# Kernel tuning notes

Measured on AMD Instinct MI355X. Metric: run time of the kernel, lower is better.

The kernel has to match this reference:

```python
import math
import jax, jax.numpy as jnp
import numpy as np

BS, N, D, H = 4, 512, 1024, 16
HD = D // H


def setup_inputs() -> dict:
    key = jax.random.key(0)
    ks = jax.random.split(key, 12)
    s = 1.0 / math.sqrt(D)
    return {
        "x": jax.random.normal(ks[0], (BS, N, D), jnp.float32),
        "r": jax.random.normal(ks[1], (BS, 3, N, N), jnp.float32),
        "bias": jax.random.normal(ks[2], (BS, H, N, N), jnp.float32),
        "mask": jax.random.randint(ks[3], (BS, 1, N, N), 0, 2, jnp.int32),
        "wq": jax.random.normal(ks[4], (D, D), jnp.float32) * s,
        "bq": jnp.zeros((D,), jnp.float32),
        "wk": jax.random.normal(ks[5], (D, D), jnp.float32) * s,
        "bk": jnp.zeros((D,), jnp.float32),
        "wv": jax.random.normal(ks[6], (D, D), jnp.float32) * s,
        "bv": jnp.zeros((D,), jnp.float32),
        "wo": jax.random.normal(ks[7], (D, 1), jnp.float32) * s,
        "bo": jnp.zeros((1,), jnp.float32),
    }


def reference(x, r, bias, mask, wq, bq, wk, bk, wv, bv, wo, bo):
    bs, n, d = x.shape
    # projections -> (bs, h, n, hd)
    q = (x @ wq + bq).reshape(bs, n, H, HD).transpose(0, 2, 1, 3)
    k = (x @ wk + bk).reshape(bs, n, H, HD).transpose(0, 2, 1, 3)
    v = (x @ wv + bv).reshape(bs, n, H, HD).transpose(0, 2, 1, 3)
    logits = jnp.einsum("bhid,bhjd->bhij", q, k) / math.sqrt(HD) + bias
    logits = jnp.where(mask == 0, jnp.float32(-1e9), logits)
    w = jax.nn.softmax(logits, axis=-1)  # (bs,h,n,n)
    # o[b,i,c,h,d] = sum_j r[b,c,i,j] * w[b,h,i,j] * v[b,h,j,d]
    o = jnp.einsum("bcij,bhij,bhjd->bichd", r, w, v)
    o = o.reshape(bs, n, 3, d)
    force = o @ wo + bo  # (bs, n, 3, 1)
    return force
```

## Files before the change

### kernel.cpp

```cpp
#include <hip/hip_runtime.h>
#include <stdint.h>

#define BSZ 4
#define NSEQ 512
#define DMOD 1024
#define NH 16
#define HD 64

typedef __attribute__((ext_vector_type(8))) short bf16x8;
typedef __attribute__((ext_vector_type(4))) float f32x4;

__device__ __forceinline__ unsigned short f2bf(float f) {
    union { float f; uint32_t u; } v; v.f = f;
    uint32_t u = v.u;
    u += 0x7FFFu + ((u >> 16) & 1u);
    return (unsigned short)(u >> 16);
}

__device__ __forceinline__ void gload_lds16(const unsigned short* g, unsigned short* l) {
    __builtin_amdgcn_global_load_lds(
        (const __attribute__((address_space(1))) void*)g,
        (__attribute__((address_space(3))) void*)l, 16, 0, 0);
}

__global__ __launch_bounds__(256) void k_prep(
        const float* __restrict__ x, const float* __restrict__ wq, const float* __restrict__ wk,
        const float* __restrict__ wv, const float* __restrict__ bv, const float* __restrict__ wo,
        unsigned short* __restrict__ xb, unsigned short* __restrict__ wqt,
        unsigned short* __restrict__ wkt, float* __restrict__ wv2t, float* __restrict__ bv2) {
    __shared__ float t[32][33];
    int bx = blockIdx.x, tid = threadIdx.x;
    if (bx < 2048) {
        int i = bx * 256 + tid;
        float4 v = ((const float4*)x)[i];
        ushort4 o; o.x = f2bf(v.x); o.y = f2bf(v.y); o.z = f2bf(v.z); o.w = f2bf(v.w);
        ((ushort4*)xb)[i] = o;
    } else if (bx < 4096) {
        int g = bx - 2048; int z = g >> 10; g &= 1023;
        const float* src = z ? wk : wq;
        unsigned short* dst = z ? wkt : wqt;
        int be = (g & 31) * 32, bc = (g >> 5) * 32;
        int tx = tid & 31, ty = tid >> 5;
        #pragma unroll
        for (int yy = 0; yy < 32; yy += 8)
            t[ty + yy][tx] = src[(size_t)(be + ty + yy) * DMOD + bc + tx];
        __syncthreads();
        #pragma unroll
        for (int yy = 0; yy < 32; yy += 8)
            dst[(size_t)(bc + ty + yy) * DMOD + be + tx] = f2bf(t[tx][ty + yy]);
    } else {
        int g = bx - 4096;
        int grp = tid >> 6, l = tid & 63;
        int e = g * 4 + grp;
        float out = 0.f;
        #pragma unroll
        for (int it = 0; it < 16; ++it) {
            float v = wv[(size_t)e * DMOD + it * 64 + l] * wo[it * 64 + l];
            #pragma unroll
            for (int off = 1; off < 64; off <<= 1) v += __shfl_xor(v, off, 64);
            if (l == it) out = v;
        }
        if (l < 16) wv2t[l * DMOD + e] = out;
        if (g == 0 && grp == 0) {
            float ob = 0.f;
            #pragma unroll
            for (int it = 0; it < 16; ++it) {
                float v = bv[it * 64 + l] * wo[it * 64 + l];
                #pragma unroll
                for (int off = 1; off < 64; off <<= 1) v += __shfl_xor(v, off, 64);
                if (l == it) ob = v;
            }
            if (l < 16) bv2[l] = ob;
        }
    }
}

__global__ __launch_bounds__(256) void k_mid(
        const float* __restrict__ x, const float* __restrict__ wv2t, const float* __restrict__ bv2,
        const unsigned short* __restrict__ xb, const unsigned short* __restrict__ wqt,
        const unsigned short* __restrict__ wkt, const float* __restrict__ bq,
        const float* __restrict__ bk, float* __restrict__ u,
        unsigned short* __restrict__ qT, unsigned short* __restrict__ kT) {
    __shared__ unsigned short lA[64 * 128];
    __shared__ unsigned short lB[64 * 128];
    int bx = blockIdx.x, tid = threadIdx.x;
    if (bx < 512) {
        int wave = bx * 4 + (tid >> 6);
        int l = tid & 63;
        int b = wave >> 9, j = wave & 511;
        const float* xr = x + (size_t)(b * NSEQ + j) * DMOD;
        float p[16];
        #pragma unroll
        for (int h = 0; h < 16; ++h) p[h] = 0.f;
        for (int it = 0; it < 16; ++it) {
            int e = l + it * 64;
            float xv = xr[e];
            #pragma unroll
            for (int h = 0; h < 16; ++h) p[h] += xv * wv2t[h * DMOD + e];
        }
        #pragma unroll
        for (int h = 0; h < 16; ++h) {
            #pragma unroll
            for (int off = 1; off < 64; off <<= 1) p[h] += __shfl_xor(p[h], off, 64);
        }
        float out = 0.f;
        #pragma unroll
        for (int h = 0; h < 16; ++h) if (l == h) out = p[h] + bv2[h];
        if (l < 16) u[(b * 16 + l) * NSEQ + j] = out;
        return;
    }
    int g = bx - 512;
    int z = g >> 9;
    const unsigned short* Wt = z ? wkt : wqt;
    const float* bias = z ? bk : bq;
    unsigned short* outT = z ? kT : qT;
    float scale = z ? 1.f : 0.125f;
    int w = tid >> 6, lane = tid & 63;
    int quad = lane >> 4, col = lane & 15;
    int m0 = (g & 31) * 64;
    int n0 = ((g >> 5) & 15) * 64;

    f32x4 acc[4];
    #pragma unroll
    for (int nt = 0; nt < 4; ++nt) acc[nt] = (f32x4){0.f, 0.f, 0.f, 0.f};

    int rl_base = lane >> 4;
    int cs = lane & 15;
    int asw = cs & 7;

    for (int kc = 0; kc < 8; ++kc) {
        int k0 = kc * 128;
        #pragma unroll
        for (int t = 0; t < 4; ++t) {
            int rl = t * 4 + rl_base;
            int row = w * 16 + rl;
            int cg = cs ^ (rl & 7);
            gload_lds16(xb + (size_t)(m0 + row) * DMOD + k0 + cg * 8,
                        &lA[(w * 16 + t * 4) * 128]);
            gload_lds16(Wt + (size_t)(n0 + row) * DMOD + k0 + cg * 8,
                        &lB[(w * 16 + t * 4) * 128]);
        }
        __syncthreads();
        int arow = w * 16 + cs;
        #pragma unroll
        for (int ks = 0; ks < 4; ++ks) {
            int blk = (ks * 4 + quad) ^ asw;
            bf16x8 af = *(const bf16x8*)&lA[arow * 128 + blk * 8];
            #pragma unroll
            for (int nt = 0; nt < 4; ++nt) {
                bf16x8 bfr = *(const bf16x8*)&lB[(nt * 16 + cs) * 128 + blk * 8];
                acc[nt] = __builtin_amdgcn_mfma_f32_16x16x32_bf16(af, bfr, acc[nt], 0, 0, 0);
            }
        }
        __syncthreads();
    }
    #pragma unroll
    for (int nt = 0; nt < 4; ++nt) {
        int n = n0 + nt * 16 + col;
        int h = n >> 6, d = n & 63;
        float bvv = bias[n];
        #pragma unroll
        for (int r = 0; r < 4; ++r) {
            int mg = m0 + w * 16 + quad * 4 + r;
            int b = mg >> 9, i = mg & 511;
            outT[(size_t)((b * 16 + h) * NSEQ + i) * HD + d] = f2bf((acc[nt][r] + bvv) * scale);
        }
    }
}

#define RSTRIDE 68
__global__ __launch_bounds__(512, 4) void k_attn(
        const unsigned short* __restrict__ qT, const unsigned short* __restrict__ kT,
        const float* __restrict__ bias, const int* __restrict__ mask,
        const float* __restrict__ u, const float* __restrict__ r,
        float* __restrict__ spart, float* __restrict__ P) {
    __shared__ float rT[3 * 16 * RSTRIDE];
    __shared__ int mT[16 * RSTRIDE];
    int tid = threadIdx.x;
    int w = tid >> 6, lane = tid & 63;
    int quad = lane >> 4, col = lane & 15;
    int it = blockIdx.x, jc = blockIdx.y, bz = blockIdx.z;
    int b = bz >> 1, hg = bz & 1;
    int i0 = it * 16, j0 = jc * 64;
    int h = hg * 8 + w;
    int bh = b * 16 + h;

    const unsigned short* qbase = qT + ((size_t)(bh * NSEQ + i0 + col)) * HD + quad * 8;
    bf16x8 a0 = *(const bf16x8*)qbase;
    bf16x8 a1 = *(const bf16x8*)(qbase + 32);

    bf16x8 kf0[4], kf1[4];
    #pragma unroll
    for (int jt = 0; jt < 4; ++jt) {
        const unsigned short* kbase = kT + ((size_t)(bh * NSEQ + j0 + jt * 16 + col)) * HD + quad * 8;
        kf0[jt] = *(const bf16x8*)kbase;
        kf1[jt] = *(const bf16x8*)(kbase + 32);
    }
    const float* brow = bias + (size_t)bh * NSEQ * NSEQ;
    float bvv[16];
    #pragma unroll
    for (int jt = 0; jt < 4; ++jt) {
        int j = j0 + jt * 16 + col;
        #pragma unroll
        for (int rr = 0; rr < 4; ++rr) {
            int i = i0 + quad * 4 + rr;
            bvv[jt * 4 + rr] = brow[(size_t)i * NSEQ + j];
        }
    }
    const float* ub = u + (size_t)bh * NSEQ;
    float uvv[4];
    #pragma unroll
    for (int jt = 0; jt < 4; ++jt) uvv[jt] = ub[j0 + jt * 16 + col];

    #pragma unroll
    for (int t = 0; t < 3; ++t) {
        int idx = t * 512 + tid;
        int c = idx >> 9, rem = idx & 511;
        int i = rem >> 5, j2 = rem & 31;
        float2 v = *(const float2*)&r[((size_t)(b * 3 + c) * NSEQ + i0 + i) * NSEQ + j0 + j2 * 2];
        *(float2*)&rT[(c * 16 + i) * RSTRIDE + j2 * 2] = v;
    }
    const int* mrow = mask + (size_t)b * NSEQ * NSEQ;
    #pragma unroll
    for (int t = 0; t < 2; ++t) {
        int idx = t * 512 + tid;
        int i = idx >> 6, j = idx & 63;
        mT[i * RSTRIDE + j] = mrow[(size_t)(i0 + i) * NSEQ + j0 + j];
    }

    asm volatile("s_waitcnt lgkmcnt(0)" ::: "memory");
    __builtin_amdgcn_sched_barrier(0);
    __builtin_amdgcn_s_barrier();
    __builtin_amdgcn_sched_barrier(0);

    float sp[4] = {0.f, 0.f, 0.f, 0.f};
    float pc0[4] = {0.f, 0.f, 0.f, 0.f};
    float pc1[4] = {0.f, 0.f, 0.f, 0.f};
    float pc2[4] = {0.f, 0.f, 0.f, 0.f};
    #pragma unroll
    for (int jt = 0; jt < 4; ++jt) {
        f32x4 acc = (f32x4){0.f, 0.f, 0.f, 0.f};
        acc = __builtin_amdgcn_mfma_f32_16x16x32_bf16(a0, kf0[jt], acc, 0, 0, 0);
        acc = __builtin_amdgcn_mfma_f32_16x16x32_bf16(a1, kf1[jt], acc, 0, 0, 0);
        float uv = uvv[jt];
        int jl = jt * 16 + col;
        #pragma unroll
        for (int rr = 0; rr < 4; ++rr) {
            int il = quad * 4 + rr;
            int mv = mT[il * RSTRIDE + jl];
            float lg = acc[rr] + bvv[jt * 4 + rr];
            float e = (mv == 0) ? 0.f : __expf(lg);
            sp[rr] += e;
            float eu = e * uv;
            pc0[rr] += eu * rT[(0 * 16 + il) * RSTRIDE + jl];
            pc1[rr] += eu * rT[(1 * 16 + il) * RSTRIDE + jl];
            pc2[rr] += eu * rT[(2 * 16 + il) * RSTRIDE + jl];
        }
    }
    #pragma unroll
    for (int rr = 0; rr < 4; ++rr) {
        #pragma unroll
        for (int off = 1; off < 16; off <<= 1) {
            sp[rr]  += __shfl_xor(sp[rr], off, 64);
            pc0[rr] += __shfl_xor(pc0[rr], off, 64);
            pc1[rr] += __shfl_xor(pc1[rr], off, 64);
            pc2[rr] += __shfl_xor(pc2[rr], off, 64);
        }
    }
    if (col == 0) {
        #pragma unroll
        for (int rr = 0; rr < 4; ++rr) {
            int il = quad * 4 + rr;
            spart[((size_t)bh * NSEQ + i0 + il) * 8 + jc] = sp[rr];
            size_t pb = ((((size_t)(b * 16 + h) * 32 + it) * 8 + jc) * 16 + il) * 3;
            P[pb + 0] = pc0[rr];
            P[pb + 1] = pc1[rr];
            P[pb + 2] = pc2[rr];
        }
    }
}

__global__ __launch_bounds__(256) void k_final(
        const float* __restrict__ spart, const float* __restrict__ P,
        const float* __restrict__ bo, float* __restrict__ out) {
    int tid = threadIdx.x;
    int rloc = tid >> 4, h = tid & 15;
    int row = blockIdx.x * 16 + rloc;
    int b = row >> 9, i = row & 511;
    int it = i >> 4, il = i & 15;
    int bh = b * 16 + h;
    const float* sprow = spart + ((size_t)bh * NSEQ + i) * 8;
    float4 sa = *(const float4*)sprow;
    float4 sb = *(const float4*)(sprow + 4);
    float s = sa.x + sa.y + sa.z + sa.w + sb.x + sb.y + sb.z + sb.w;
    float sinv = (s > 0.f) ? 1.f / s : 0.f;
    float f0 = 0.f, f1 = 0.f, f2 = 0.f;
    #pragma unroll
    for (int jc = 0; jc < 8; ++jc) {
        size_t pb = ((((size_t)(b * 16 + h) * 32 + it) * 8 + jc) * 16 + il) * 3;
        f0 += P[pb]; f1 += P[pb + 1]; f2 += P[pb + 2];
    }
    f0 *= sinv; f1 *= sinv; f2 *= sinv;
    #pragma unroll
    for (int off = 1; off < 16; off <<= 1) {
        f0 += __shfl_xor(f0, off, 64);
        f1 += __shfl_xor(f1, off, 64);
        f2 += __shfl_xor(f2, off, 64);
    }
    if (h == 0) {
        float bov = bo[0];
        out[(size_t)row * 3 + 0] = f0 + bov;
        out[(size_t)row * 3 + 1] = f1 + bov;
        out[(size_t)row * 3 + 2] = f2 + bov;
    }
}

extern "C" void kernel_launch(void* const* d_in, const int* in_sizes, int n_in,
                              void* d_out, int out_size, void* d_ws, size_t ws_size,
                              hipStream_t stream) {
    const float* x    = (const float*)d_in[0];
    const float* rr   = (const float*)d_in[1];
    const float* bias = (const float*)d_in[2];
    const int*   mask = (const int*)d_in[3];
    const float* wq   = (const float*)d_in[4];
    const float* bq   = (const float*)d_in[5];
    const float* wk   = (const float*)d_in[6];
    const float* bk   = (const float*)d_in[7];
    const float* wv   = (const float*)d_in[8];
    const float* bv   = (const float*)d_in[9];
    const float* wo   = (const float*)d_in[10];
    const float* bo   = (const float*)d_in[11];
    float* out = (float*)d_out;

    char* ws = (char*)d_ws;
    unsigned short* xb    = (unsigned short*)(ws + 0);
    unsigned short* wqt   = (unsigned short*)(ws + 4194304);
    unsigned short* wkt   = (unsigned short*)(ws + 6291456);
    float*          wv2t  = (float*)(ws + 8388608);
    float*          bv2   = (float*)(ws + 8454144);
    float*          u     = (float*)(ws + 8454400);
    unsigned short* qT    = (unsigned short*)(ws + 8585472);
    unsigned short* kT    = (unsigned short*)(ws + 12779776);
    float*          spart = (float*)(ws + 16974080);
    float*          P     = (float*)(ws + 18022656);

    k_prep<<<4352, 256, 0, stream>>>(x, wq, wk, wv, bv, wo, xb, wqt, wkt, wv2t, bv2);
    k_mid<<<1536, 256, 0, stream>>>(x, wv2t, bv2, xb, wqt, wkt, bq, bk, u, qT, kT);
    k_attn<<<dim3(32, 8, 8), 512, 0, stream>>>(qT, kT, bias, mask, u, rr, spart, P);
    k_final<<<128, 256, 0, stream>>>(spart, P, bo, out);
}
```

Baseline: 188.5 us.

## Enlarge QK GEMM tiles, pack r/mask into LDS float4, reorder partial layout

The Q/K projection GEMM moves from 64x64 to 128x128 block tiles with a 4x4 MFMA grid per wave and 64-wide K chunks, and GEMM blocks now come first in the grid. This raises data reuse per LDS load and cuts the number of blocks. The attention kernel loads r and mask into registers early and packs them into one interleaved float4 LDS array, turning the mask select into a multiply, and loads bias with nontemporal hints. The partial-sum layout is reordered so the final kernel can read it with float4 loads and reduce across heads through LDS. The larger register footprint may lower occupancy.

```diff
diff --git a/kernel.cpp b/kernel.cpp
--- a/kernel.cpp
+++ b/kernel.cpp
@@ -75,17 +75,17 @@
     }
 }
 
-__global__ __launch_bounds__(256) void k_mid(
+__global__ __launch_bounds__(256, 3) void k_mid(
         const float* __restrict__ x, const float* __restrict__ wv2t, const float* __restrict__ bv2,
         const unsigned short* __restrict__ xb, const unsigned short* __restrict__ wqt,
         const unsigned short* __restrict__ wkt, const float* __restrict__ bq,
         const float* __restrict__ bk, float* __restrict__ u,
         unsigned short* __restrict__ qT, unsigned short* __restrict__ kT) {
-    __shared__ unsigned short lA[64 * 128];
-    __shared__ unsigned short lB[64 * 128];
+    __shared__ unsigned short lA[128 * 64];
+    __shared__ unsigned short lB[128 * 64];
     int bx = blockIdx.x, tid = threadIdx.x;
-    if (bx < 512) {
-        int wave = bx * 4 + (tid >> 6);
+    if (bx >= 256) {
+        int wave = (bx - 256) * 4 + (tid >> 6);
         int l = tid & 63;
         int b = wave >> 9, j = wave & 511;
         const float* xr = x + (size_t)(b * NSEQ + j) * DMOD;
@@ -109,73 +109,84 @@
         if (l < 16) u[(b * 16 + l) * NSEQ + j] = out;
         return;
     }
-    int g = bx - 512;
-    int z = g >> 9;
+    int g = bx;
+    int mt = g & 15, nt8 = (g >> 4) & 7, z = g >> 7;
     const unsigned short* Wt = z ? wkt : wqt;
     const float* bias = z ? bk : bq;
     unsigned short* outT = z ? kT : qT;
     float scale = z ? 1.f : 0.125f;
+    int m0 = mt * 128, n0 = nt8 * 128;
     int w = tid >> 6, lane = tid & 63;
-    int quad = lane >> 4, col = lane & 15;
-    int m0 = (g & 31) * 64;
-    int n0 = ((g >> 5) & 15) * 64;
-
-    f32x4 acc[4];
-    #pragma unroll
-    for (int nt = 0; nt < 4; ++nt) acc[nt] = (f32x4){0.f, 0.f, 0.f, 0.f};
-
-    int rl_base = lane >> 4;
-    int cs = lane & 15;
-    int asw = cs & 7;
-
-    for (int kc = 0; kc < 8; ++kc) {
-        int k0 = kc * 128;
-        #pragma unroll
-        for (int t = 0; t < 4; ++t) {
-            int rl = t * 4 + rl_base;
-            int row = w * 16 + rl;
-            int cg = cs ^ (rl & 7);
-            gload_lds16(xb + (size_t)(m0 + row) * DMOD + k0 + cg * 8,
-                        &lA[(w * 16 + t * 4) * 128]);
-            gload_lds16(Wt + (size_t)(n0 + row) * DMOD + k0 + cg * 8,
-                        &lB[(w * 16 + t * 4) * 128]);
+    int wr = w >> 1, wc = w & 1;
+    int quad = lane >> 4, cs = lane & 15;
+    int l8 = lane >> 3, l7 = lane & 7;
+    int sg = l7 ^ l8;
+
+    f32x4 acc[4][4];
+    #pragma unroll
+    for (int mi = 0; mi < 4; ++mi)
+        #pragma unroll
+        for (int ni = 0; ni < 4; ++ni) acc[mi][ni] = (f32x4){0.f, 0.f, 0.f, 0.f};
+
+    for (int kc = 0; kc < 16; ++kc) {
+        int k0 = kc * 64;
+        #pragma unroll
+        for (int q = 0; q < 4; ++q) {
+            int row = w * 32 + q * 8 + l8;
+            gload_lds16(xb + (size_t)(m0 + row) * DMOD + k0 + sg * 8,
+                        &lA[(w * 32 + q * 8) * 64]);
+            gload_lds16(Wt + (size_t)(n0 + row) * DMOD + k0 + sg * 8,
+                        &lB[(w * 32 + q * 8) * 64]);
         }
         __syncthreads();
-        int arow = w * 16 + cs;
-        #pragma unroll
-        for (int ks = 0; ks < 4; ++ks) {
-            int blk = (ks * 4 + quad) ^ asw;
-            bf16x8 af = *(const bf16x8*)&lA[arow * 128 + blk * 8];
-            #pragma unroll
-            for (int nt = 0; nt < 4; ++nt) {
-                bf16x8 bfr = *(const bf16x8*)&lB[(nt * 16 + cs) * 128 + blk * 8];
-                acc[nt] = __builtin_amdgcn_mfma_f32_16x16x32_bf16(af, bfr, acc[nt], 0, 0, 0);
+        #pragma unroll
+        for (int ks = 0; ks < 2; ++ks) {
+            bf16x8 af[4], bfr[4];
+            #pragma unroll
+            for (int mi = 0; mi < 4; ++mi) {
+                int row = wr * 64 + mi * 16 + cs;
+                int gq = (ks * 4 + quad) ^ (row & 7);
+                af[mi] = *(const bf16x8*)&lA[row * 64 + gq * 8];
             }
+            #pragma unroll
+            for (int ni = 0; ni < 4; ++ni) {
+                int row = wc * 64 + ni * 16 + cs;
+                int gq = (ks * 4 + quad) ^ (row & 7);
+                bfr[ni] = *(const bf16x8*)&lB[row * 64 + gq * 8];
+            }
+            #pragma unroll
+            for (int mi = 0; mi < 4; ++mi)
+                #pragma unroll
+                for (int ni = 0; ni < 4; ++ni)
+                    acc[mi][ni] = __builtin_amdgcn_mfma_f32_16x16x32_bf16(
+                        af[mi], bfr[ni], acc[mi][ni], 0, 0, 0);
         }
         __syncthreads();
     }
     #pragma unroll
-    for (int nt = 0; nt < 4; ++nt) {
-        int n = n0 + nt * 16 + col;
+    for (int ni = 0; ni < 4; ++ni) {
+        int n = n0 + wc * 64 + ni * 16 + cs;
         int h = n >> 6, d = n & 63;
         float bvv = bias[n];
         #pragma unroll
-        for (int r = 0; r < 4; ++r) {
-            int mg = m0 + w * 16 + quad * 4 + r;
-            int b = mg >> 9, i = mg & 511;
-            outT[(size_t)((b * 16 + h) * NSEQ + i) * HD + d] = f2bf((acc[nt][r] + bvv) * scale);
-        }
-    }
-}
-
-#define RSTRIDE 68
+        for (int mi = 0; mi < 4; ++mi) {
+            #pragma unroll
+            for (int rr = 0; rr < 4; ++rr) {
+                int mg = m0 + wr * 64 + mi * 16 + quad * 4 + rr;
+                int b = mg >> 9, i = mg & 511;
+                outT[(size_t)((b * 16 + h) * NSEQ + i) * HD + d] =
+                    f2bf((acc[mi][ni][rr] + bvv) * scale);
+            }
+        }
+    }
+}
+
 __global__ __launch_bounds__(512, 4) void k_attn(
         const unsigned short* __restrict__ qT, const unsigned short* __restrict__ kT,
         const float* __restrict__ bias, const int* __restrict__ mask,
         const float* __restrict__ u, const float* __restrict__ r,
         float* __restrict__ spart, float* __restrict__ P) {
-    __shared__ float rT[3 * 16 * RSTRIDE];
-    __shared__ int mT[16 * RSTRIDE];
+    __shared__ float rT4[16 * 64 * 4];
     int tid = threadIdx.x;
     int w = tid >> 6, lane = tid & 63;
     int quad = lane >> 4, col = lane & 15;
@@ -185,6 +196,20 @@
     int h = hg * 8 + w;
     int bh = b * 16 + h;
 
+    float sr0[2], sr1[2], sr2[2], smf[2];
+    const float* rbase = r + (size_t)b * 3 * NSEQ * NSEQ;
+    const int* mrow = mask + (size_t)b * NSEQ * NSEQ;
+    #pragma unroll
+    for (int t = 0; t < 2; ++t) {
+        int slot = t * 512 + tid;
+        int il = slot >> 6, jl = slot & 63;
+        size_t off = (size_t)(i0 + il) * NSEQ + j0 + jl;
+        sr0[t] = rbase[off];
+        sr1[t] = rbase[(size_t)NSEQ * NSEQ + off];
+        sr2[t] = rbase[2 * (size_t)NSEQ * NSEQ + off];
+        smf[t] = (float)mrow[off];
+    }
+
     const unsigned short* qbase = qT + ((size_t)(bh * NSEQ + i0 + col)) * HD + quad * 8;
     bf16x8 a0 = *(const bf16x8*)qbase;
     bf16x8 a1 = *(const bf16x8*)(qbase + 32);
@@ -204,7 +229,7 @@
         #pragma unroll
         for (int rr = 0; rr < 4; ++rr) {
             int i = i0 + quad * 4 + rr;
-            bvv[jt * 4 + rr] = brow[(size_t)i * NSEQ + j];
+            bvv[jt * 4 + rr] = __builtin_nontemporal_load(&brow[(size_t)i * NSEQ + j]);
         }
     }
     const float* ub = u + (size_t)bh * NSEQ;
@@ -213,19 +238,10 @@
     for (int jt = 0; jt < 4; ++jt) uvv[jt] = ub[j0 + jt * 16 + col];
 
     #pragma unroll
-    for (int t = 0; t < 3; ++t) {
-        int idx = t * 512 + tid;
-        int c = idx >> 9, rem = idx & 511;
-        int i = rem >> 5, j2 = rem & 31;
-        float2 v = *(const float2*)&r[((size_t)(b * 3 + c) * NSEQ + i0 + i) * NSEQ + j0 + j2 * 2];
-        *(float2*)&rT[(c * 16 + i) * RSTRIDE + j2 * 2] = v;
-    }
-    const int* mrow = mask + (size_t)b * NSEQ * NSEQ;
-    #pragma unroll
     for (int t = 0; t < 2; ++t) {
-        int idx = t * 512 + tid;
-        int i = idx >> 6, j = idx & 63;
-        mT[i * RSTRIDE + j] = mrow[(size_t)(i0 + i) * NSEQ + j0 + j];
+        int slot = t * 512 + tid;
+        float4 pk; pk.x = sr0[t]; pk.y = sr1[t]; pk.z = sr2[t]; pk.w = smf[t];
+        *(float4*)&rT4[slot * 4] = pk;
     }
 
     asm volatile("s_waitcnt lgkmcnt(0)" ::: "memory");
@@ -247,14 +263,14 @@
         #pragma unroll
         for (int rr = 0; rr < 4; ++rr) {
             int il = quad * 4 + rr;
-            int mv = mT[il * RSTRIDE + jl];
+            float4 v = *(const float4*)&rT4[(il * 64 + jl) * 4];
             float lg = acc[rr] + bvv[jt * 4 + rr];
-            float e = (mv == 0) ? 0.f : __expf(lg);
+            float e = __expf(lg) * v.w;
             sp[rr] += e;
             float eu = e * uv;
-            pc0[rr] += eu * rT[(0 * 16 + il) * RSTRIDE + jl];
-            pc1[rr] += eu * rT[(1 * 16 + il) * RSTRIDE + jl];
-            pc2[rr] += eu * rT[(2 * 16 + il) * RSTRIDE + jl];
+            pc0[rr] += eu * v.x;
+            pc1[rr] += eu * v.y;
+            pc2[rr] += eu * v.z;
         }
     }
     #pragma unroll
@@ -272,7 +288,7 @@
         for (int rr = 0; rr < 4; ++rr) {
             int il = quad * 4 + rr;
             spart[((size_t)bh * NSEQ + i0 + il) * 8 + jc] = sp[rr];
-            size_t pb = ((((size_t)(b * 16 + h) * 32 + it) * 8 + jc) * 16 + il) * 3;
+            size_t pb = ((((size_t)bh * 32 + it) * 16 + il) * 8 + jc) * 3;
             P[pb + 0] = pc0[rr];
             P[pb + 1] = pc1[rr];
             P[pb + 2] = pc2[rr];
@@ -283,35 +299,48 @@
 __global__ __launch_bounds__(256) void k_final(
         const float* __restrict__ spart, const float* __restrict__ P,
         const float* __restrict__ bo, float* __restrict__ out) {
+    __shared__ float part[4][16][3];
+    int bx = blockIdx.x;
+    int b = bx >> 5, it = bx & 31;
     int tid = threadIdx.x;
-    int rloc = tid >> 4, h = tid & 15;
-    int row = blockIdx.x * 16 + rloc;
-    int b = row >> 9, i = row & 511;
-    int it = i >> 4, il = i & 15;
+    int il = tid & 15, h = tid >> 4;
+    int w = tid >> 6;
     int bh = b * 16 + h;
+    int i = it * 16 + il;
     const float* sprow = spart + ((size_t)bh * NSEQ + i) * 8;
     float4 sa = *(const float4*)sprow;
     float4 sb = *(const float4*)(sprow + 4);
     float s = sa.x + sa.y + sa.z + sa.w + sb.x + sb.y + sb.z + sb.w;
     float sinv = (s > 0.f) ? 1.f / s : 0.f;
-    float f0 = 0.f, f1 = 0.f, f2 = 0.f;
-    #pragma unroll
-    for (int jc = 0; jc < 8; ++jc) {
-        size_t pb = ((((size_t)(b * 16 + h) * 32 + it) * 8 + jc) * 16 + il) * 3;
-        f0 += P[pb]; f1 += P[pb + 1]; f2 += P[pb + 2];
-    }
-    f0 *= sinv; f1 *= sinv; f2 *= sinv;
-    #pragma unroll
-    for (int off = 1; off < 16; off <<= 1) {
-        f0 += __shfl_xor(f0, off, 64);
-        f1 += __shfl_xor(f1, off, 64);
-        f2 += __shfl_xor(f2, off, 64);
-    }
-    if (h == 0) {
+    const float* pbase = P + (((size_t)bh * 32 + it) * 16 + il) * 24;
+    float f[3] = {0.f, 0.f, 0.f};
+    #pragma unroll
+    for (int q = 0; q < 6; ++q) {
+        float4 v = *(const float4*)(pbase + q * 4);
+        f[(q * 4 + 0) % 3] += v.x;
+        f[(q * 4 + 1) % 3] += v.y;
+        f[(q * 4 + 2) % 3] += v.z;
+        f[(q * 4 + 3) % 3] += v.w;
+    }
+    f[0] *= sinv; f[1] *= sinv; f[2] *= sinv;
+    #pragma unroll
+    for (int c = 0; c < 3; ++c) {
+        f[c] += __shfl_xor(f[c], 16, 64);
+        f[c] += __shfl_xor(f[c], 32, 64);
+    }
+    if ((tid & 48) == 0) {
+        part[w][il][0] = f[0]; part[w][il][1] = f[1]; part[w][il][2] = f[2];
+    }
+    __syncthreads();
+    if (tid < 16) {
         float bov = bo[0];
-        out[(size_t)row * 3 + 0] = f0 + bov;
-        out[(size_t)row * 3 + 1] = f1 + bov;
-        out[(size_t)row * 3 + 2] = f2 + bov;
+        float o0 = part[0][tid][0] + part[1][tid][0] + part[2][tid][0] + part[3][tid][0];
+        float o1 = part[0][tid][1] + part[1][tid][1] + part[2][tid][1] + part[3][tid][1];
+        float o2 = part[0][tid][2] + part[1][tid][2] + part[2][tid][2] + part[3][tid][2];
+        size_t row = (size_t)b * NSEQ + it * 16 + tid;
+        out[row * 3 + 0] = o0 + bov;
+        out[row * 3 + 1] = o1 + bov;
+        out[row * 3 + 2] = o2 + bov;
     }
 }
 
@@ -345,7 +374,7 @@
     float*          P     = (float*)(ws + 18022656);
 
     k_prep<<<4352, 256, 0, stream>>>(x, wq, wk, wv, bv, wo, xb, wqt, wkt, wv2t, bv2);
-    k_mid<<<1536, 256, 0, stream>>>(x, wv2t, bv2, xb, wqt, wkt, bq, bk, u, qT, kT);
+    k_mid<<<768, 256, 0, stream>>>(x, wv2t, bv2, xb, wqt, wkt, bq, bk, u, qT, kT);
     k_attn<<<dim3(32, 8, 8), 512, 0, stream>>>(qT, kT, bias, mask, u, rr, spart, P);
     k_final<<<128, 256, 0, stream>>>(spart, P, bo, out);
 }
```

Result: no change. 191.1 us (+1.4%).
